# Kernel tuning notes

Measured on AMD Instinct MI355X. Metric: run time of the kernel, lower is better.

## Reference

```python
import jax, jax.numpy as jnp
import numpy as np

B, S, D, H = 4, 2048, 256, 8  # batch, seq (context=target), hidden_dim, n_heads


def setup_inputs() -> dict:
    key = jax.random.key(0)
    ks = jax.random.split(key, 12)
    sd = 1.0 / np.sqrt(D)          # torch Linear default init scale (uniform bound)
    sdo = 1.0 / np.sqrt(H * D)
    inp = {
        "k": jax.random.normal(ks[0], (B, S, D), jnp.float32),
        "v": jax.random.normal(ks[1], (B, S, D), jnp.float32),
        "q": jax.random.normal(ks[2], (B, S, D), jnp.float32),
        # Per-head projection weights, stacked over heads. Stored so y = x @ W + b.
        "Wk": jax.random.uniform(ks[3], (H, D, D), jnp.float32, -sd, sd),
        "bk": jax.random.uniform(ks[4], (H, D), jnp.float32, -sd, sd),
        "Wv": jax.random.uniform(ks[5], (H, D, D), jnp.float32, -sd, sd),
        "bv": jax.random.uniform(ks[6], (H, D), jnp.float32, -sd, sd),
        "Wq": jax.random.uniform(ks[7], (H, D, D), jnp.float32, -sd, sd),
        "bq": jax.random.uniform(ks[8], (H, D), jnp.float32, -sd, sd),
        # Final mixing Linear: input is heads interleaved as (hidden, head) flattened,
        # i.e. input index = hid * H + head (torch stack(dim=-1).view order).
        "Wo": jax.random.uniform(ks[9], (H * D, D), jnp.float32, -sdo, sdo),
        "bo": jax.random.uniform(ks[10], (D,), jnp.float32, -sdo, sdo),
    }
    return inp


def reference(k, v, q, Wk, bk, Wv, bv, Wq, bq, Wo, bo):
    # Per-head linear projections (batched over heads instead of a Python loop)
    k_ = jnp.einsum('bmd,hde->bhme', k, Wk) + bk[None, :, None, :]  # [B,H,S,D]
    v_ = jnp.einsum('bmd,hde->bhme', v, Wv) + bv[None, :, None, :]
    q_ = jnp.einsum('bnd,hde->bhne', q, Wq) + bq[None, :, None, :]
    scale = jnp.asarray(np.sqrt(D), k.dtype)
    # dot attention: scores[b,h,n,m] = <q_n, k_m> / sqrt(D); softmax over keys m
    scores = jnp.einsum('bhnd,bhmd->bhnm', q_, k_) / scale
    w = jax.nn.softmax(scores, axis=-1)
    rep = jnp.einsum('bhnm,bhmd->bhnd', w, v_)  # [B,H,S,D]
    # torch: stack(heads, dim=-1) -> [B,S,D,H], then view -> [B,S,D*H] (hid-major)
    outs = rep.transpose(0, 2, 3, 1).reshape(rep.shape[0], rep.shape[2], -1)
    return outs @ Wo + bo
```

## Files before the change

kernel.cpp:

```cpp
#include <hip/hip_runtime.h>

#define BB 4
#define SS 2048
#define DD 256
#define HH 8

typedef unsigned short u16;
typedef __attribute__((ext_vector_type(8))) short bf16x8;
typedef __attribute__((ext_vector_type(4))) float f32x4;
typedef __attribute__((ext_vector_type(16))) float f32x16;
typedef __attribute__((ext_vector_type(4))) short s16x4;

__device__ __forceinline__ f32x4 MFMA(bf16x8 a, bf16x8 b, f32x4 c) {
    return __builtin_amdgcn_mfma_f32_16x16x32_bf16(a, b, c, 0, 0, 0);
}
__device__ __forceinline__ f32x16 MFMA32(bf16x8 a, bf16x8 b, f32x16 c) {
    return __builtin_amdgcn_mfma_f32_32x32x16_bf16(a, b, c, 0, 0, 0);
}

__device__ __forceinline__ u16 f2bf_rtn(float x) {
    unsigned u = __float_as_uint(x);
    u += 0x7FFFu + ((u >> 16) & 1u);
    return (u16)(u >> 16);
}
__device__ __forceinline__ float bf2f(u16 h) {
    return __uint_as_float(((unsigned)h) << 16);
}
__device__ __forceinline__ void split2(float x, u16 &hi, u16 &lo) {
    hi = f2bf_rtn(x);
    lo = f2bf_rtn(x - bf2f(hi));
}

__device__ __forceinline__ void gl_lds16(const u16* g, u16* l) {
    __builtin_amdgcn_global_load_lds(
        (const __attribute__((address_space(1))) unsigned int*)(g),
        (__attribute__((address_space(3))) unsigned int*)(l), 16, 0, 0);
}

__global__ void prep_a(const float* __restrict__ x, u16* __restrict__ hi) {
    int r = blockIdx.x;
    int d = threadIdx.x;
    hi[(size_t)r * 256 + d] = f2bf_rtn(x[(size_t)r * 256 + d]);
}

__global__ void prep_w(const float* __restrict__ W, u16* __restrict__ Whi,
                       u16* __restrict__ Wlo) {
    int n = blockIdx.x;
    int h = n >> 8, e = n & 255;
    int d = threadIdx.x;
    float x = W[((size_t)h * 256 + d) * 256 + e];
    u16 hi, lo; split2(x, hi, lo);
    Whi[(size_t)n * 256 + d] = hi;
    Wlo[(size_t)n * 256 + d] = lo;
}

__global__ void prep_wo(const float* __restrict__ W, u16* __restrict__ Whi,
                        u16* __restrict__ Wlo) {
    int n = blockIdx.x;
    for (int k = threadIdx.x; k < 2048; k += 256) {
        int d = k & 255, h = k >> 8;
        float x = W[((size_t)(d * 8 + h)) * 256 + n];
        u16 hi, lo; split2(x, hi, lo);
        Whi[(size_t)n * 2048 + k] = hi;
        Wlo[(size_t)n * 2048 + k] = lo;
    }
}

template<int MODE, int AMODE, int TERMS, int BN>
__global__ __launch_bounds__(512, 2) void gemm_split(
    const u16* __restrict__ Ahi, const u16* __restrict__ Alo,
    const u16* __restrict__ Bhi, const u16* __restrict__ Blo,
    const float* __restrict__ bias,
    u16* __restrict__ Ohi,
    float* __restrict__ Of,
    int M, int N, int K, float scale)
{
    constexpr int WN = (BN == 128) ? 4 : 2;
    constexpr int WM = 8 / WN;
    constexpr int MSUB = (128 / WM) / 16;
    constexpr int NSUB = (BN / WN) / 16;
    constexpr int NPL = (TERMS == 3) ? 4 : (TERMS == 2) ? 3 : 2;

    __shared__ u16 lds[2 * NPL * 4096];

    const int tid = threadIdx.x;
    const int lane = tid & 63, wave = tid >> 6;
    const int wm = wave / WN, wn = wave % WN;
    const int m0 = blockIdx.y * 128, n0 = blockIdx.x * BN;

    f32x4 acc[MSUB][NSUB];
#pragma unroll
    for (int i = 0; i < MSUB; ++i)
#pragma unroll
        for (int j = 0; j < NSUB; ++j) acc[i][j] = {0.f, 0.f, 0.f, 0.f};

    const int rho = tid >> 2;
    const int Xs = (tid & 3) << 3;
    const int ldsW = wave * 512;

#define G_ISSUE(k0v, p)                                                         \
    {   u16* Bse = lds + (p) * (NPL * 4096);                                    \
        size_t ga;                                                              \
        if (AMODE == 0)                                                         \
            ga = (size_t)(m0 + rho) * K + (k0v) + Xs;                           \
        else                                                                    \
            ga = ((size_t)((m0 >> 11) * 8 + ((k0v) >> 8)) * SS                  \
                  + (m0 & 2047) + rho) * DD + ((k0v) & 255) + Xs;               \
        gl_lds16(Ahi + ga, Bse + ldsW);                                         \
        if (TERMS == 3) gl_lds16(Alo + ga, Bse + 3 * 4096 + ldsW);              \
        if (BN == 128 || tid < 256) {                                           \
            size_t gb = (size_t)(n0 + rho) * K + (k0v) + Xs;                    \
            gl_lds16(Bhi + gb, Bse + 1 * 4096 + ldsW);                          \
            if (TERMS >= 2) gl_lds16(Blo + gb, Bse + 2 * 4096 + ldsW);          \
        }                                                                       \
    }

    const int NK = K >> 5;
    G_ISSUE(0, 0);
    __syncthreads();

    for (int kt = 0; kt < NK; ++kt) {
        if (kt < NK - 1) G_ISSUE((kt + 1) << 5, (kt + 1) & 1);

        const u16* Bse = lds + (kt & 1) * (NPL * 4096);
        const int g8 = (lane >> 4) << 3;
        const int rA = wm * (128 / WM), rB = wn * (BN / WN);
        bf16x8 bh[NSUB], bl[NSUB];
#pragma unroll
        for (int ns = 0; ns < NSUB; ++ns) {
            const int rb = rB + ns * 16 + (lane & 15);
            bh[ns] = *(const bf16x8*)(Bse + 1 * 4096 + rb * 32 + g8);
            if (TERMS >= 2) bl[ns] = *(const bf16x8*)(Bse + 2 * 4096 + rb * 32 + g8);
        }
#pragma unroll
        for (int ms = 0; ms < MSUB; ++ms) {
            const int ra = rA + ms * 16 + (lane & 15);
            bf16x8 ah = *(const bf16x8*)(Bse + ra * 32 + g8);
            bf16x8 al;
            if (TERMS == 3) al = *(const bf16x8*)(Bse + 3 * 4096 + ra * 32 + g8);
#pragma unroll
            for (int ns = 0; ns < NSUB; ++ns) {
                acc[ms][ns] = MFMA(ah, bh[ns], acc[ms][ns]);
                if (TERMS == 3) acc[ms][ns] = MFMA(al, bh[ns], acc[ms][ns]);
                if (TERMS >= 2) acc[ms][ns] = MFMA(ah, bl[ns], acc[ms][ns]);
            }
        }
        __syncthreads();
    }
#undef G_ISSUE

#pragma unroll
    for (int ms = 0; ms < MSUB; ++ms)
#pragma unroll
        for (int ns = 0; ns < NSUB; ++ns)
#pragma unroll
            for (int r = 0; r < 4; ++r) {
                int row = m0 + wm * (128 / WM) + ms * 16 + (lane >> 4) * 4 + r;
                int col = n0 + wn * (BN / WN) + ns * 16 + (lane & 15);
                float v = (acc[ms][ns][r] + bias[col]) * scale;
                if (MODE == 2) {
                    Of[(size_t)row * N + col] = v;
                } else {
                    int b = row >> 11, s = row & 2047, hh = col >> 8, e = col & 255;
                    size_t idx;
                    if (MODE == 0)
                        idx = ((size_t)(b * HH + hh) * SS + s) * DD + e;
                    else
                        idx = ((size_t)(b * HH + hh) * DD + e) * SS + s;
                    Ohi[idx] = f2bf_rtn(v);
                }
            }
}

__global__ __launch_bounds__(512, 2) void attn_kernel(
    const u16* __restrict__ Qhi,
    const u16* __restrict__ Khi,
    const u16* __restrict__ Vhi,
    u16* __restrict__ Rhi, u16* __restrict__ Rlo)
{
    __shared__ u16 lK[3][8192];
    __shared__ u16 lV[3][8192];

    const int tid = threadIdx.x, lane = tid & 63, wave = tid >> 6;
    const int qc = lane & 31, g2 = lane >> 5;
    const int wg = ((blockIdx.x & 7) << 5) + (blockIdx.x >> 3);
    const int bh = wg >> 3;
    const int qt = wg & 7;
    const size_t base = (size_t)bh * SS * DD;
    const int q0w = qt * 256 + wave * 32;

    bf16x8 qB[16];
#pragma unroll
    for (int ks = 0; ks < 16; ++ks)
        qB[ks] = *(const bf16x8*)(Qhi + base + (size_t)(q0w + qc) * DD + ks * 16 + g2 * 8);

    int koff[2], voff[2];
#pragma unroll
    for (int i = 0; i < 2; ++i) {
        const int s = tid + i * 512;
        const int kr = s >> 5, kX = s & 31;
        const int kap = (kr & 0x13) | ((kr & 4) << 1) | ((kr & 8) >> 1);
        koff[i] = kap * DD + ((kX ^ kr) << 3);
        const int ve = s >> 2, vXs = s & 3;
        voff[i] = ve * SS + (((vXs ^ ((ve >> 3) & 3))) << 3);
    }

    float l_part = 0.f;
    f32x16 acc[8];
#pragma unroll
    for (int ec = 0; ec < 8; ++ec) acc[ec] = {};

#define ISSUE(tt, p)                                                            \
    {   const u16* Kg = Khi + base + (size_t)(tt) * 32 * DD;                    \
        const u16* Vg = Vhi + base + (size_t)(tt) * 32;                         \
        u16* Kb = &lK[p][0]; u16* Vb = &lV[p][0];                               \
        gl_lds16(Kg + koff[0], Kb + wave * 512);                                \
        gl_lds16(Kg + koff[1], Kb + wave * 512 + 4096);                         \
        gl_lds16(Vg + voff[0], Vb + wave * 512);                                \
        gl_lds16(Vg + voff[1], Vb + wave * 512 + 4096);                         \
    }

    ISSUE(0, 0);
    ISSUE(1, 1);

    for (int t = 0; t < 64; ++t) {
        if (t < 63) { asm volatile("s_waitcnt vmcnt(4)" ::: "memory"); }
        else        { asm volatile("s_waitcnt vmcnt(0)" ::: "memory"); }
        __builtin_amdgcn_sched_barrier(0);
        __builtin_amdgcn_s_barrier();
        __builtin_amdgcn_sched_barrier(0);

        if (t + 2 < 64) ISSUE(t + 2, (t + 2) % 3);

        const u16* Kb = &lK[t % 3][0];
        const u16* Vb = &lV[t % 3][0];

        f32x16 sa = {}, sb = {};
        __builtin_amdgcn_s_setprio(1);
#pragma unroll
        for (int ks = 0; ks < 8; ++ks) {
            bf16x8 ka = *(const bf16x8*)(Kb + qc * DD + (((2 * ks + g2) ^ qc) << 3));
            bf16x8 kb2 = *(const bf16x8*)(Kb + qc * DD + (((2 * (ks + 8) + g2) ^ qc) << 3));
            sa = MFMA32(ka, qB[ks], sa);
            sb = MFMA32(kb2, qB[ks + 8], sb);
        }
        __builtin_amdgcn_s_setprio(0);

        f32x16 s = sa + sb;
#pragma unroll
        for (int n = 0; n < 16; ++n) s[n] = __builtin_amdgcn_exp2f(s[n] - 8.0f);
        float tl = 0.f;
#pragma unroll
        for (int n = 0; n < 16; ++n) tl += s[n];
        l_part += tl;

        bf16x8 p0, p1;
#pragma unroll
        for (int j = 0; j < 8; ++j) p0[j] = (short)f2bf_rtn(s[j]);
#pragma unroll
        for (int j = 0; j < 8; ++j) p1[j] = (short)f2bf_rtn(s[8 + j]);

        __builtin_amdgcn_s_setprio(1);
#pragma unroll
        for (int ec = 0; ec < 8; ++ec) {
            const int e = ec * 32 + qc;
            bf16x8 v0 = *(const bf16x8*)(Vb + e * 32 + (((g2 ^ ((e >> 3) & 3))) << 3));
            bf16x8 v1 = *(const bf16x8*)(Vb + e * 32 + ((((2 + g2) ^ ((e >> 3) & 3))) << 3));
            acc[ec] = MFMA32(v0, p0, acc[ec]);
            acc[ec] = MFMA32(v1, p1, acc[ec]);
        }
        __builtin_amdgcn_s_setprio(0);
    }
#undef ISSUE

    float l = l_part + __shfl_xor(l_part, 32);
    float inv = 1.0f / l;
    const size_t rowbase = ((size_t)bh * SS + q0w + qc) * DD;
#pragma unroll
    for (int ec = 0; ec < 8; ++ec)
#pragma unroll
        for (int rr = 0; rr < 4; ++rr) {
            const int e0 = ec * 32 + 8 * rr + 4 * g2;
            s16x4 hv, lv;
#pragma unroll
            for (int j = 0; j < 4; ++j) {
                u16 h2, l2; split2(acc[ec][4 * rr + j] * inv, h2, l2);
                hv[j] = (short)h2; lv[j] = (short)l2;
            }
            *(s16x4*)(Rhi + rowbase + e0) = hv;
            *(s16x4*)(Rlo + rowbase + e0) = lv;
        }
}

extern "C" void kernel_launch(void* const* d_in, const int* in_sizes, int n_in,
                              void* d_out, int out_size, void* d_ws, size_t ws_size,
                              hipStream_t stream)
{
    (void)in_sizes; (void)n_in; (void)out_size; (void)ws_size;
    const float* k_in = (const float*)d_in[0];
    const float* v_in = (const float*)d_in[1];
    const float* q_in = (const float*)d_in[2];
    const float* Wk   = (const float*)d_in[3];
    const float* bk   = (const float*)d_in[4];
    const float* Wv   = (const float*)d_in[5];
    const float* bv   = (const float*)d_in[6];
    const float* Wq   = (const float*)d_in[7];
    const float* bq   = (const float*)d_in[8];
    const float* Wo   = (const float*)d_in[9];
    const float* bo   = (const float*)d_in[10];
    float* out = (float*)d_out;

    char* p = (char*)d_ws;
    const size_t MB = 1024 * 1024;
    u16* WqH = (u16*)(p + 0 * MB);
    u16* WqL = (u16*)(p + 1 * MB);
    u16* WkH = (u16*)(p + 2 * MB);
    u16* WkL = (u16*)(p + 3 * MB);
    u16* WvH = (u16*)(p + 4 * MB);
    u16* WvL = (u16*)(p + 5 * MB);
    u16* WoH = (u16*)(p + 6 * MB);
    u16* WoL = (u16*)(p + 7 * MB);
    const size_t PB = 32 * MB;
    u16* QH  = (u16*)(p + 8 * MB);
    u16* KH  = (u16*)(p + 8 * MB + 1 * PB);
    u16* VTH = (u16*)(p + 8 * MB + 2 * PB);
    u16* RH  = (u16*)(p + 8 * MB + 3 * PB);
    u16* RL  = (u16*)(p + 8 * MB + 4 * PB);
    u16* AqH = (u16*)(p + 168 * MB);
    u16* AkH = (u16*)(p + 172 * MB);
    u16* AvH = (u16*)(p + 176 * MB);

    prep_a<<<dim3(8192), dim3(256), 0, stream>>>(q_in, AqH);
    prep_a<<<dim3(8192), dim3(256), 0, stream>>>(k_in, AkH);
    prep_a<<<dim3(8192), dim3(256), 0, stream>>>(v_in, AvH);
    prep_w<<<dim3(2048), dim3(256), 0, stream>>>(Wq, WqH, WqL);
    prep_w<<<dim3(2048), dim3(256), 0, stream>>>(Wk, WkH, WkL);
    prep_w<<<dim3(2048), dim3(256), 0, stream>>>(Wv, WvH, WvL);
    prep_wo<<<dim3(256), dim3(256), 0, stream>>>(Wo, WoH, WoL);

    const float qscale = 1.4426950408889634f / 16.0f;
    gemm_split<0, 0, 1, 128><<<dim3(16, 64), dim3(512), 0, stream>>>(
        AqH, nullptr, WqH, WqL, bq, QH, nullptr, 8192, 2048, 256, qscale);
    gemm_split<0, 0, 1, 128><<<dim3(16, 64), dim3(512), 0, stream>>>(
        AkH, nullptr, WkH, WkL, bk, KH, nullptr, 8192, 2048, 256, 1.0f);
    gemm_split<1, 0, 2, 128><<<dim3(16, 64), dim3(512), 0, stream>>>(
        AvH, nullptr, WvH, WvL, bv, VTH, nullptr, 8192, 2048, 256, 1.0f);

    attn_kernel<<<dim3(256), dim3(512), 0, stream>>>(
        QH, KH, VTH, RH, RL);

    gemm_split<2, 2, 3, 64><<<dim3(4, 64), dim3(512), 0, stream>>>(
        RH, RL, WoH, WoL, bo, nullptr, out, 8192, 256, 2048, 1.0f);
}
```

Measured before the change: 313.8 us.

## Software-pipeline attention loop: overlap QK of tile t with PV of tile t-1

Restructures the attention main loop so each iteration runs the QK^T MFMAs for tile t, then the PV MFMAs for tile t-1 (using probabilities kept in registers), then softmax for tile t. This lets the exp and packing work be hidden behind independent matrix work. LDS buffering goes from 3 to 4 stages so the V tile of t-1 stays valid while new loads are issued. It also replaces round-to-nearest bf16 conversion with truncation, which is cheaper but slightly less accurate. The larger LDS footprint (128KB per block) may reduce occupancy below the two blocks per CU that launch_bounds requests.

```diff
diff --git a/kernel.cpp b/kernel.cpp
--- a/kernel.cpp
+++ b/kernel.cpp
@@ -178,8 +178,8 @@
     const u16* __restrict__ Vhi,
     u16* __restrict__ Rhi, u16* __restrict__ Rlo)
 {
-    __shared__ u16 lK[3][8192];
-    __shared__ u16 lV[3][8192];
+    __shared__ u16 lK[4][8192];
+    __shared__ u16 lV[4][8192];
 
     const int tid = threadIdx.x, lane = tid & 63, wave = tid >> 6;
     const int qc = lane & 31, g2 = lane >> 5;
@@ -213,65 +213,90 @@
 #define ISSUE(tt, p)                                                            \
     {   const u16* Kg = Khi + base + (size_t)(tt) * 32 * DD;                    \
         const u16* Vg = Vhi + base + (size_t)(tt) * 32;                         \
-        u16* Kb = &lK[p][0]; u16* Vb = &lV[p][0];                               \
-        gl_lds16(Kg + koff[0], Kb + wave * 512);                                \
-        gl_lds16(Kg + koff[1], Kb + wave * 512 + 4096);                         \
-        gl_lds16(Vg + voff[0], Vb + wave * 512);                                \
-        gl_lds16(Vg + voff[1], Vb + wave * 512 + 4096);                         \
-    }
+        u16* Kb_ = &lK[p][0]; u16* Vb_ = &lV[p][0];                             \
+        gl_lds16(Kg + koff[0], Kb_ + wave * 512);                               \
+        gl_lds16(Kg + koff[1], Kb_ + wave * 512 + 4096);                        \
+        gl_lds16(Vg + voff[0], Vb_ + wave * 512);                               \
+        gl_lds16(Vg + voff[1], Vb_ + wave * 512 + 4096);                        \
+    }
+
+#define QK_T(Kb)                                                                \
+    {   __builtin_amdgcn_s_setprio(1);                                          \
+        _Pragma("unroll")                                                       \
+        for (int ks = 0; ks < 8; ++ks) {                                        \
+            bf16x8 ka = *(const bf16x8*)((Kb) + qc * DD + (((2 * ks + g2) ^ qc) << 3)); \
+            bf16x8 kb2 = *(const bf16x8*)((Kb) + qc * DD + (((2 * (ks + 8) + g2) ^ qc) << 3)); \
+            sa = MFMA32(ka, qB[ks], sa);                                        \
+            sb = MFMA32(kb2, qB[ks + 8], sb);                                   \
+        }                                                                       \
+        __builtin_amdgcn_s_setprio(0);  }
+
+#define SM_T()                                                                  \
+    {   f32x16 s = sa + sb;                                                     \
+        _Pragma("unroll")                                                       \
+        for (int n = 0; n < 16; ++n) s[n] = __builtin_amdgcn_exp2f(s[n] - 8.0f); \
+        float tl = 0.f;                                                         \
+        _Pragma("unroll")                                                       \
+        for (int n = 0; n < 16; ++n) tl += s[n];                                \
+        l_part += tl;                                                           \
+        _Pragma("unroll")                                                       \
+        for (int j = 0; j < 4; ++j) {                                           \
+            unsigned a = __float_as_uint(s[2 * j]);                             \
+            unsigned b = __float_as_uint(s[2 * j + 1]);                         \
+            ((unsigned*)&pb0)[j] = (a >> 16) | (b & 0xffff0000u);               \
+            unsigned c = __float_as_uint(s[8 + 2 * j]);                         \
+            unsigned d = __float_as_uint(s[8 + 2 * j + 1]);                     \
+            ((unsigned*)&pb1)[j] = (c >> 16) | (d & 0xffff0000u);               \
+        }  }
+
+#define PV_T(Vb)                                                                \
+    {   __builtin_amdgcn_s_setprio(1);                                          \
+        _Pragma("unroll")                                                       \
+        for (int ec = 0; ec < 8; ++ec) {                                        \
+            const int e = ec * 32 + qc;                                         \
+            bf16x8 v0 = *(const bf16x8*)((Vb) + e * 32 + (((g2 ^ ((e >> 3) & 3))) << 3)); \
+            bf16x8 v1 = *(const bf16x8*)((Vb) + e * 32 + ((((2 + g2) ^ ((e >> 3) & 3))) << 3)); \
+            acc[ec] = MFMA32(v0, pb0, acc[ec]);                                 \
+            acc[ec] = MFMA32(v1, pb1, acc[ec]);                                 \
+        }                                                                       \
+        __builtin_amdgcn_s_setprio(0);  }
+
+    bf16x8 pb0, pb1;
+    f32x16 sa, sb;
 
     ISSUE(0, 0);
     ISSUE(1, 1);
-
-    for (int t = 0; t < 64; ++t) {
+    asm volatile("s_waitcnt vmcnt(4)" ::: "memory");
+    __builtin_amdgcn_sched_barrier(0);
+    __builtin_amdgcn_s_barrier();
+    __builtin_amdgcn_sched_barrier(0);
+    ISSUE(2, 2);
+    sa = {}; sb = {};
+    QK_T(&lK[0][0]);
+    SM_T();
+
+    for (int t = 1; t < 64; ++t) {
         if (t < 63) { asm volatile("s_waitcnt vmcnt(4)" ::: "memory"); }
         else        { asm volatile("s_waitcnt vmcnt(0)" ::: "memory"); }
         __builtin_amdgcn_sched_barrier(0);
         __builtin_amdgcn_s_barrier();
         __builtin_amdgcn_sched_barrier(0);
 
-        if (t + 2 < 64) ISSUE(t + 2, (t + 2) % 3);
-
-        const u16* Kb = &lK[t % 3][0];
-        const u16* Vb = &lV[t % 3][0];
-
-        f32x16 sa = {}, sb = {};
-        __builtin_amdgcn_s_setprio(1);
-#pragma unroll
-        for (int ks = 0; ks < 8; ++ks) {
-            bf16x8 ka = *(const bf16x8*)(Kb + qc * DD + (((2 * ks + g2) ^ qc) << 3));
-            bf16x8 kb2 = *(const bf16x8*)(Kb + qc * DD + (((2 * (ks + 8) + g2) ^ qc) << 3));
-            sa = MFMA32(ka, qB[ks], sa);
-            sb = MFMA32(kb2, qB[ks + 8], sb);
-        }
-        __builtin_amdgcn_s_setprio(0);
-
-        f32x16 s = sa + sb;
-#pragma unroll
-        for (int n = 0; n < 16; ++n) s[n] = __builtin_amdgcn_exp2f(s[n] - 8.0f);
-        float tl = 0.f;
-#pragma unroll
-        for (int n = 0; n < 16; ++n) tl += s[n];
-        l_part += tl;
-
-        bf16x8 p0, p1;
-#pragma unroll
-        for (int j = 0; j < 8; ++j) p0[j] = (short)f2bf_rtn(s[j]);
-#pragma unroll
-        for (int j = 0; j < 8; ++j) p1[j] = (short)f2bf_rtn(s[8 + j]);
-
-        __builtin_amdgcn_s_setprio(1);
-#pragma unroll
-        for (int ec = 0; ec < 8; ++ec) {
-            const int e = ec * 32 + qc;
-            bf16x8 v0 = *(const bf16x8*)(Vb + e * 32 + (((g2 ^ ((e >> 3) & 3))) << 3));
-            bf16x8 v1 = *(const bf16x8*)(Vb + e * 32 + ((((2 + g2) ^ ((e >> 3) & 3))) << 3));
-            acc[ec] = MFMA32(v0, p0, acc[ec]);
-            acc[ec] = MFMA32(v1, p1, acc[ec]);
-        }
-        __builtin_amdgcn_s_setprio(0);
-    }
+        if (t + 2 < 64) ISSUE(t + 2, (t + 2) & 3);
+
+        const u16* Kb = &lK[t & 3][0];
+        const u16* Vp = &lV[(t - 1) & 3][0];
+
+        sa = {}; sb = {};
+        QK_T(Kb);
+        PV_T(Vp);
+        SM_T();
+    }
+    PV_T(&lV[3][0]);
 #undef ISSUE
+#undef QK_T
+#undef SM_T
+#undef PV_T
 
     float l = l_part + __shfl_xor(l_part, 32);
     float inv = 1.0f / l;
```

After: 497.9 us. +58.7%, slower.
